# Optimization experiments

Hardware: AMD Instinct MI355X
Metric: run time of the kernel (lower is better)

## Reference

```python
import jax, jax.numpy as jnp
import numpy as np

EPS = 1e-5  # torch BatchNorm1d default eps


def _batchnorm(x, gamma, beta):
    # training-mode BatchNorm1d: biased batch statistics over the N dim
    mean = jnp.mean(x, axis=0)
    var = jnp.var(x, axis=0)
    return (x - mean) * jax.lax.rsqrt(var + EPS) * gamma + beta


def setup_inputs() -> dict:
    key = jax.random.key(0)
    ks = jax.random.split(key, 12)
    N_last, N_cur, E, F = 100000, 50000, 500000, 300
    Din = F + 3  # 303: neighbor features concat coord delta
    inp = {
        "last_coors": jax.random.normal(ks[0], (N_last, 3), jnp.float32),
        "last_features": jax.random.normal(ks[1], (N_last, F), jnp.float32),
        "current_coors": jax.random.normal(ks[2], (N_cur, 3), jnp.float32),
        "cur_idx": jax.random.randint(ks[3], (E,), 0, N_cur),
        "last_idx": jax.random.randint(ks[4], (E,), 0, N_last),
        # in_linear: Linear(303,300) + ReLU + BN(300)
        "W1": jax.random.normal(ks[5], (Din, F), jnp.float32) / np.sqrt(Din),
        "b1": jnp.zeros((F,), jnp.float32),
        "g1": jnp.ones((F,), jnp.float32),
        "be1": jnp.zeros((F,), jnp.float32),
        # out_linear: Linear(300,300) + ReLU + BN(300)
        "W2": jax.random.normal(ks[6], (F, F), jnp.float32) / np.sqrt(F),
        "b2": jnp.zeros((F,), jnp.float32),
        "g2": jnp.ones((F,), jnp.float32),
        "be2": jnp.zeros((F,), jnp.float32),
    }
    return inp


def reference(last_coors, last_features, current_coors, cur_idx, last_idx,
              W1, b1, g1, be1, W2, b2, g2, be2):
    N_cur = current_coors.shape[0]
    # gather: neighbor features + (neighbor - center) coordinate deltas -> [E, 303]
    edge_feats = jnp.concatenate(
        [last_features[last_idx], last_coors[last_idx] - current_coors[cur_idx]],
        axis=1)
    # in_linear MLP on edges
    h = _batchnorm(jnp.maximum(edge_feats @ W1 + b1, 0.0), g1, be1)  # [E, 300]
    # scatter-max aggregation to current-level nodes (empty segments -> 0,
    # matching torch_scatter.scatter(..., reduce='max') zero-init behavior)
    agg = jax.ops.segment_max(h, cur_idx, num_segments=N_cur)  # [N_cur, 300]
    agg = jnp.where(jnp.isfinite(agg), agg, 0.0)
    # out_linear MLP on nodes
    out = _batchnorm(jnp.maximum(agg @ W2 + b2, 0.0), g2, be2)
    return out
```

## Files before the change

kernel.cpp:

```cpp
#include <hip/hip_runtime.h>
#include <hip/hip_bf16.h>


#define NPART 64
#define SB 256
#define SEGB 32
#define CHS 256
#define UNR 8

typedef __bf16 bf16_t;
typedef __bf16 bf16x8 __attribute__((ext_vector_type(8)));
typedef float f32x4 __attribute__((ext_vector_type(4)));

__global__ void hist_k(const int* __restrict__ ci, int E, int* __restrict__ hist)
{
    const int e = blockIdx.x * 256 + threadIdx.x;
    if (e < E) atomicAdd(&hist[ci[e]], 1);
}

__global__ void scan_reduce(const int* __restrict__ hist, int nseg, int* __restrict__ bsum)
{
    __shared__ int s[SB];
    const int tid = threadIdx.x;
    const int i = blockIdx.x * SB + tid;
    s[tid] = (i < nseg) ? hist[i] : 0;
    __syncthreads();
    for (int o = SB / 2; o > 0; o >>= 1) {
        if (tid < o) s[tid] += s[tid + o];
        __syncthreads();
    }
    if (tid == 0) bsum[blockIdx.x] = s[0];
}

__global__ void scan_top(int* __restrict__ bsum, int nb)
{
    __shared__ int s[SB];
    const int tid = threadIdx.x;
    const int v = (tid < nb) ? bsum[tid] : 0;
    s[tid] = v;
    __syncthreads();
    for (int o = 1; o < SB; o <<= 1) {
        int x = 0;
        if (tid >= o) x = s[tid - o];
        __syncthreads();
        s[tid] += x;
        __syncthreads();
    }
    if (tid < nb) bsum[tid] = s[tid] - v;
}

__global__ void scan_final(const int* __restrict__ hist, int nseg,
                           const int* __restrict__ bsum, int* __restrict__ cnt)
{
    __shared__ int s[SB];
    const int tid = threadIdx.x;
    const int i = blockIdx.x * SB + tid;
    const int v = (i < nseg) ? hist[i] : 0;
    s[tid] = v;
    __syncthreads();
    for (int o = 1; o < SB; o <<= 1) {
        int x = 0;
        if (tid >= o) x = s[tid - o];
        __syncthreads();
        s[tid] += x;
        __syncthreads();
    }
    if (i < nseg) cnt[i] = s[tid] - v + bsum[blockIdx.x];
}

__global__ void scatter_k(const int* __restrict__ ci, const int* __restrict__ li,
                          int E, int* __restrict__ cnt, int2* __restrict__ sorted)
{
    const int e = blockIdx.x * 256 + threadIdx.x;
    if (e >= E) return;
    const int c = ci[e];
    const int pos = atomicAdd(&cnt[c], 1);
    sorted[pos] = make_int2(li[e], c);
}

__global__ void pack_wt2(const float* __restrict__ W1, const float* __restrict__ W2,
                         bf16_t* __restrict__ WT)
{
    const int idx = blockIdx.x * 256 + threadIdx.x;
    if (idx >= 2 * 384 * 320) return;
    const int w = idx / (384 * 320);
    const int rem = idx - w * (384 * 320);
    const int n = rem / 320, k = rem % 320;
    const float* W = w ? W2 : W1;
    float v = (n < 300 && k < 300) ? W[k * 300 + n] : 0.f;
    WT[idx] = (bf16_t)v;
}

template<int MODE>
__launch_bounds__(512, 4)
__global__ void gemm_mfma(const float* __restrict__ A32, int M,
                          const int* __restrict__ segEnd,
                          const float* __restrict__ ac,
                          const bf16_t* __restrict__ WT,
                          const float* __restrict__ bias,
                          bf16_t* __restrict__ outBF,
                          float* __restrict__ outF,
                          float* __restrict__ part)
{
    __shared__ bf16_t As[128][72];
    __shared__ bf16_t Bs[320][72];
    __shared__ float sSum[320], sSq[320];
    __shared__ float sAc[640];

    const int tid  = threadIdx.x;
    const int lane = tid & 63, wv = tid >> 6;
    const int wm = wv & 1, wn = wv >> 1;
    const int m0 = blockIdx.x * 128;
    const int rl = lane & 15, quad = lane >> 4;

    if (MODE == 1) {
        if (tid < 320) { sSum[tid] = 0.f; sSq[tid] = 0.f; }
        for (int i = tid; i < 640; i += 512) sAc[i] = ac[i];
    }

    const int kcT = (tid & 7) * 8;
    const int rT  = tid >> 3;
    int growA[2]; bool emp[2];
    #pragma unroll
    for (int i = 0; i < 2; ++i) {
        growA[i] = min(m0 + i * 64 + rT, M - 1);
        emp[i] = false;
        if (MODE == 1)
            emp[i] = segEnd[growA[i]] == (growA[i] ? segEnd[growA[i] - 1] : 0);
    }

    f32x4 acc[4][5];
    #pragma unroll
    for (int i = 0; i < 4; ++i)
        #pragma unroll
        for (int j = 0; j < 5; ++j)
            acc[i][j] = (f32x4){0.f, 0.f, 0.f, 0.f};

    if (MODE == 1) __syncthreads();

    for (int k0 = 0; k0 < 320; k0 += 64) {
        const int c0 = k0 + kcT;

        float4 la[2], lb[2];
        #pragma unroll
        for (int i = 0; i < 2; ++i) {
            la[i] = make_float4(0.f, 0.f, 0.f, 0.f);
            lb[i] = make_float4(0.f, 0.f, 0.f, 0.f);
            if (MODE == 0) {
                if (c0 + 8 <= 300) {
                    la[i] = *reinterpret_cast<const float4*>(&A32[(long)growA[i] * 300 + c0]);
                    lb[i] = *reinterpret_cast<const float4*>(&A32[(long)growA[i] * 300 + c0 + 4]);
                } else if (c0 < 300) {
                    la[i] = *reinterpret_cast<const float4*>(&A32[(long)growA[i] * 300 + c0]);
                }
            } else {
                la[i] = *reinterpret_cast<const float4*>(&A32[(long)growA[i] * 320 + c0]);
                lb[i] = *reinterpret_cast<const float4*>(&A32[(long)growA[i] * 320 + c0 + 4]);
            }
        }
        bf16x8 wb[5];
        #pragma unroll
        for (int i = 0; i < 5; ++i)
            wb[i] = *reinterpret_cast<const bf16x8*>(&WT[(long)(i * 64 + rT) * 320 + c0]);

        #pragma unroll
        for (int i = 0; i < 2; ++i) {
            bf16x8 v;
            if (MODE == 0) {
                v = (bf16x8){(bf16_t)la[i].x, (bf16_t)la[i].y, (bf16_t)la[i].z, (bf16_t)la[i].w,
                             (bf16_t)lb[i].x, (bf16_t)lb[i].y, (bf16_t)lb[i].z, (bf16_t)lb[i].w};
            } else {
                const float4 aa = *reinterpret_cast<const float4*>(&sAc[c0]);
                const float4 ab = *reinterpret_cast<const float4*>(&sAc[c0 + 4]);
                const float4 ca = *reinterpret_cast<const float4*>(&sAc[320 + c0]);
                const float4 cb = *reinterpret_cast<const float4*>(&sAc[320 + c0 + 4]);
                const float t0 = emp[i] ? 0.f : fabsf(aa.x) * la[i].x + ca.x;
                const float t1 = emp[i] ? 0.f : fabsf(aa.y) * la[i].y + ca.y;
                const float t2 = emp[i] ? 0.f : fabsf(aa.z) * la[i].z + ca.z;
                const float t3 = emp[i] ? 0.f : fabsf(aa.w) * la[i].w + ca.w;
                const float t4 = emp[i] ? 0.f : fabsf(ab.x) * lb[i].x + cb.x;
                const float t5 = emp[i] ? 0.f : fabsf(ab.y) * lb[i].y + cb.y;
                const float t6 = emp[i] ? 0.f : fabsf(ab.z) * lb[i].z + cb.z;
                const float t7 = emp[i] ? 0.f : fabsf(ab.w) * lb[i].w + cb.w;
                v = (bf16x8){(bf16_t)t0, (bf16_t)t1, (bf16_t)t2, (bf16_t)t3,
                             (bf16_t)t4, (bf16_t)t5, (bf16_t)t6, (bf16_t)t7};
            }
            *reinterpret_cast<bf16x8*>(&As[i * 64 + rT][kcT]) = v;
        }
        #pragma unroll
        for (int i = 0; i < 5; ++i)
            *reinterpret_cast<bf16x8*>(&Bs[i * 64 + rT][kcT]) = wb[i];
        __syncthreads();

        #pragma unroll
        for (int kk = 0; kk < 2; ++kk) {
            const int kb = kk * 32 + quad * 8;
            bf16x8 af[4], bfr[5];
            #pragma unroll
            for (int mi = 0; mi < 4; ++mi)
                af[mi] = *reinterpret_cast<const bf16x8*>(&As[wm * 64 + mi * 16 + rl][kb]);
            #pragma unroll
            for (int nj = 0; nj < 5; ++nj)
                bfr[nj] = *reinterpret_cast<const bf16x8*>(&Bs[wn * 80 + nj * 16 + rl][kb]);
            #pragma unroll
            for (int mi = 0; mi < 4; ++mi)
                #pragma unroll
                for (int nj = 0; nj < 5; ++nj)
                    acc[mi][nj] = __builtin_amdgcn_mfma_f32_16x16x32_bf16(
                        af[mi], bfr[nj], acc[mi][nj], 0, 0, 0);
        }
        __syncthreads();
    }

    if (MODE == 0) {
        #pragma unroll
        for (int mi = 0; mi < 4; ++mi)
            #pragma unroll
            for (int nj = 0; nj < 5; ++nj)
                #pragma unroll
                for (int reg = 0; reg < 4; ++reg) {
                    const int r = m0 + wm * 64 + mi * 16 + quad * 4 + reg;
                    const int c = wn * 80 + nj * 16 + rl;
                    if (r < M) {
                        const float v = (c < 300) ? (acc[mi][nj][reg] + bias[c]) : 0.f;
                        outBF[(long)r * 320 + c] = (bf16_t)v;
                    }
                }
    } else {
        float csum[5] = {}, csq[5] = {};
        #pragma unroll
        for (int mi = 0; mi < 4; ++mi)
            #pragma unroll
            for (int nj = 0; nj < 5; ++nj)
                #pragma unroll
                for (int reg = 0; reg < 4; ++reg) {
                    const int r = m0 + wm * 64 + mi * 16 + quad * 4 + reg;
                    const int c = wn * 80 + nj * 16 + rl;
                    if (r < M && c < 300) {
                        float v = fmaxf(acc[mi][nj][reg] + bias[c], 0.f);
                        outF[(long)r * 300 + c] = v;
                        csum[nj] += v; csq[nj] += v * v;
                    }
                }
        #pragma unroll
        for (int nj = 0; nj < 5; ++nj) {
            const int cl = wn * 80 + nj * 16 + rl;
            if (cl < 300) {
                atomicAdd(&sSum[cl], csum[nj]);
                atomicAdd(&sSq[cl], csq[nj]);
            }
        }
        __syncthreads();
        const int slot = blockIdx.x & (NPART - 1);
        if (tid < 300) {
            atomicAdd(&part[slot * 600 + tid], sSum[tid]);
            atomicAdd(&part[slot * 600 + 300 + tid], sSq[tid]);
        }
    }
}

__launch_bounds__(320)
__global__ void edge_pass(const bf16_t* __restrict__ Gb,
                          const float* __restrict__ last_coors,
                          const float* __restrict__ cur_coors,
                          const int2* __restrict__ sorted,
                          const int*  __restrict__ segEnd,
                          const float* __restrict__ Wc,
                          const float* __restrict__ g1,
                          float* __restrict__ zbuf,
                          float* __restrict__ part1,
                          int N_cur)
{
    __shared__ int sRow[2][CHS], sCi[2][CHS];
    __shared__ float sD0[2][CHS], sD1[2][CHS], sD2[2][CHS];

    const int tid = threadIdx.x;
    const int st  = (tid >= 160) ? 1 : 0;
    const int ts  = tid - st * 160;

    const int g0   = blockIdx.x * SEGB;
    const int gEnd = min(g0 + SEGB, N_cur);
    const int gMid = min(g0 + SEGB / 2, gEnd);

    const int e00 = (g0   == 0) ? 0 : segEnd[g0 - 1];
    const int e01 = (gMid == 0) ? 0 : segEnd[gMid - 1];
    const int e11 = (gEnd == 0) ? 0 : segEnd[gEnd - 1];

    const int ebeg = st ? e01 : e00;
    const int eend = st ? e11 : e01;

    const int nch0 = (e01 - e00 + CHS - 1) / CHS;
    const int nch1 = (e11 - e01 + CHS - 1) / CHS;
    const int nch  = max(nch0, nch1);

    const int ft = ts * 2;
    const bool real = (ft < 300);
    float w00 = 0.f, w01 = 0.f, w10 = 0.f, w11 = 0.f, w20 = 0.f, w21 = 0.f;
    float sgn0 = 1.f, sgn1 = 1.f;
    if (real) {
        w00 = Wc[ft];        w01 = Wc[ft + 1];
        w10 = Wc[300 + ft];  w11 = Wc[300 + ft + 1];
        w20 = Wc[600 + ft];  w21 = Wc[600 + ft + 1];
        sgn0 = (g1[ft]     < 0.f) ? -1.f : 1.f;
        sgn1 = (g1[ft + 1] < 0.f) ? -1.f : 1.f;
    }

    int cur = -1;
    float m0 = -3.4e38f, m1 = -3.4e38f;
    float sum0 = 0.f, sq0 = 0.f, sum1 = 0.f, sq1 = 0.f;

    for (int ch = 0; ch < nch; ++ch) {
        const int cbeg = ebeg + ch * CHS;
        const int ccnt = min(CHS, eend - cbeg);

        for (int i = ts; i < ccnt; i += 160) {
            const int2 r = sorted[cbeg + i];
            sRow[st][i] = r.x * 320;
            sCi[st][i]  = r.y;
            sD0[st][i] = last_coors[r.x * 3 + 0] - cur_coors[r.y * 3 + 0];
            sD1[st][i] = last_coors[r.x * 3 + 1] - cur_coors[r.y * 3 + 1];
            sD2[st][i] = last_coors[r.x * 3 + 2] - cur_coors[r.y * 3 + 2];
        }
        __syncthreads();

        int i = 0;
        for (; i + UNR <= ccnt; i += UNR) {
            unsigned gu[UNR];
            #pragma unroll
            for (int j = 0; j < UNR; ++j)
                gu[j] = *reinterpret_cast<const unsigned*>(&Gb[(long)sRow[st][i + j] + ft]);
            #pragma unroll
            for (int j = 0; j < UNR; ++j) {
                const int ci = sCi[st][i + j];
                if (ci != cur) {
                    if (cur >= 0)
                        *reinterpret_cast<float2*>(&zbuf[(long)cur * 320 + ft]) =
                            make_float2(m0, m1);
                    cur = ci;
                    m0 = -3.4e38f; m1 = -3.4e38f;
                }
                const float gx = __uint_as_float(gu[j] << 16);
                const float gy = __uint_as_float(gu[j] & 0xffff0000u);
                const float d0 = sD0[st][i + j], d1 = sD1[st][i + j], d2 = sD2[st][i + j];
                const float y0 = fmaxf(gx + d0 * w00 + d1 * w10 + d2 * w20, 0.f);
                const float y1 = fmaxf(gy + d0 * w01 + d1 * w11 + d2 * w21, 0.f);
                sum0 += y0; sq0 += y0 * y0; m0 = fmaxf(m0, sgn0 * y0);
                sum1 += y1; sq1 += y1 * y1; m1 = fmaxf(m1, sgn1 * y1);
            }
        }
        for (; i < ccnt; ++i) {
            const int ci = sCi[st][i];
            if (ci != cur) {
                if (cur >= 0)
                    *reinterpret_cast<float2*>(&zbuf[(long)cur * 320 + ft]) =
                        make_float2(m0, m1);
                cur = ci;
                m0 = -3.4e38f; m1 = -3.4e38f;
            }
            const unsigned gu = *reinterpret_cast<const unsigned*>(&Gb[(long)sRow[st][i] + ft]);
            const float gx = __uint_as_float(gu << 16);
            const float gy = __uint_as_float(gu & 0xffff0000u);
            const float d0 = sD0[st][i], d1 = sD1[st][i], d2 = sD2[st][i];
            const float y0 = fmaxf(gx + d0 * w00 + d1 * w10 + d2 * w20, 0.f);
            const float y1 = fmaxf(gy + d0 * w01 + d1 * w11 + d2 * w21, 0.f);
            sum0 += y0; sq0 += y0 * y0; m0 = fmaxf(m0, sgn0 * y0);
            sum1 += y1; sq1 += y1 * y1; m1 = fmaxf(m1, sgn1 * y1);
        }
        __syncthreads();
    }
    if (cur >= 0)
        *reinterpret_cast<float2*>(&zbuf[(long)cur * 320 + ft]) = make_float2(m0, m1);

    const int slot = blockIdx.x & (NPART - 1);
    if (real) {
        atomicAdd(&part1[slot * 600 + ft],           sum0);
        atomicAdd(&part1[slot * 600 + ft + 1],       sum1);
        atomicAdd(&part1[slot * 600 + 300 + ft],     sq0);
        atomicAdd(&part1[slot * 600 + 300 + ft + 1], sq1);
    }
}

__global__ void stats_finalize(const float* __restrict__ part,
                               const float* __restrict__ g,
                               const float* __restrict__ be,
                               float invCnt, float* __restrict__ ac)
{
    const int t = threadIdx.x;
    if (t >= 300) {
        if (t < 320) { ac[t] = 0.f; ac[320 + t] = 0.f; }
        return;
    }
    float sum = 0.f, sq = 0.f;
    for (int p = 0; p < NPART; ++p) {
        sum += part[p * 600 + t];
        sq  += part[p * 600 + 300 + t];
    }
    const float mean = sum * invCnt;
    const float var = fmaxf(sq * invCnt - mean * mean, 0.f);
    const float inv = rsqrtf(var + 1e-5f);
    const float a = g[t] * inv;
    ac[t] = a;
    ac[320 + t] = be[t] - mean * a;
}

__global__ void finalize_out(float* __restrict__ out,
                             const float* __restrict__ ac2)
{
    const int t = threadIdx.x;
    if (t >= 300) return;
    const long i = (long)blockIdx.x * 300 + t;
    out[i] = ac2[t] * out[i] + ac2[320 + t];
}

extern "C" void kernel_launch(void* const* d_in, const int* in_sizes, int n_in,
                              void* d_out, int out_size, void* d_ws, size_t ws_size,
                              hipStream_t stream)
{
    const float* last_coors    = (const float*)d_in[0];
    const float* last_features = (const float*)d_in[1];
    const float* cur_coors     = (const float*)d_in[2];
    const int*   cur_idx       = (const int*)d_in[3];
    const int*   last_idx      = (const int*)d_in[4];
    const float* W1  = (const float*)d_in[5];
    const float* b1  = (const float*)d_in[6];
    const float* g1  = (const float*)d_in[7];
    const float* be1 = (const float*)d_in[8];
    const float* W2  = (const float*)d_in[9];
    const float* b2  = (const float*)d_in[10];
    const float* g2  = (const float*)d_in[11];
    const float* be2 = (const float*)d_in[12];
    float* out = (float*)d_out;

    const int N_last = in_sizes[0] / 3;
    const int N_cur  = in_sizes[2] / 3;
    const int E      = in_sizes[3];

    const int nb1 = (N_cur + SB - 1) / SB;

    char* ws = (char*)d_ws;
    size_t off = 0;
    bf16_t* Gb = (bf16_t*)(ws + off);  off += (size_t)N_last * 320 * 2;
    off = (off + 255) & ~(size_t)255;
    float* zbuf = (float*)(ws + off);  off += (size_t)N_cur * 320 * 4;
    off = (off + 255) & ~(size_t)255;
    int2* sorted = (int2*)(ws + off);  off += (size_t)E * 8;
    int* hist = (int*)(ws + off);      off += (size_t)nb1 * SB * 4;
    int* cnt  = (int*)(ws + off);      off += (size_t)nb1 * SB * 4;
    int* bsum = (int*)(ws + off);      off += 256 * 4;
    bf16_t* WT1 = (bf16_t*)(ws + off); off += (size_t)384 * 320 * 2;
    bf16_t* WT2 = (bf16_t*)(ws + off); off += (size_t)384 * 320 * 2;
    float* part1 = (float*)(ws + off); off += (size_t)NPART * 600 * 4;
    float* part2 = (float*)(ws + off); off += (size_t)NPART * 600 * 4;
    float* ac1   = (float*)(ws + off); off += 640 * 4;
    float* ac2   = (float*)(ws + off); off += 640 * 4;

    hipMemsetAsync(hist, 0, (size_t)nb1 * SB * 4, stream);
    hipMemsetAsync(part1, 0, (size_t)2 * NPART * 600 * 4, stream);

    hist_k<<<(E + 255) / 256, 256, 0, stream>>>(cur_idx, E, hist);
    scan_reduce<<<nb1, SB, 0, stream>>>(hist, N_cur, bsum);
    scan_top<<<1, SB, 0, stream>>>(bsum, nb1);
    scan_final<<<nb1, SB, 0, stream>>>(hist, N_cur, bsum, cnt);
    scatter_k<<<(E + 255) / 256, 256, 0, stream>>>(cur_idx, last_idx, E, cnt, sorted);

    pack_wt2<<<960, 256, 0, stream>>>(W1, W2, WT1);

    gemm_mfma<0><<<(N_last + 127) / 128, 512, 0, stream>>>(
        last_features, N_last, nullptr, nullptr, WT1, b1, Gb, nullptr, nullptr);

    const int nSB = (N_cur + SEGB - 1) / SEGB;
    edge_pass<<<nSB, 320, 0, stream>>>(Gb, last_coors, cur_coors, sorted, cnt,
                                       W1 + 300 * 300, g1, zbuf, part1, N_cur);

    stats_finalize<<<1, 320, 0, stream>>>(part1, g1, be1, 1.0f / (float)E, ac1);

    gemm_mfma<1><<<(N_cur + 127) / 128, 512, 0, stream>>>(
        zbuf, N_cur, cnt, ac1, WT2, b2, nullptr, out, part2);

    stats_finalize<<<1, 320, 0, stream>>>(part2, g2, be2, 1.0f / (float)N_cur, ac2);
    finalize_out<<<N_cur, 320, 0, stream>>>(out, ac2);
}
```

Baseline: 548.2 us.

## Double-buffer A tiles and read weights directly from global in MFMA GEMM

The GEMM kernel is restructured to 256-thread blocks covering 64 rows. Each of the 4 waves owns 80 output columns. The weight (B) tile is no longer staged in shared memory; each wave loads its B fragments straight from global/L2 memory. The A tile is double-buffered so the next k-slice's global loads overlap the current MFMA work. This removes the large Bs shared buffer and one barrier stage per iteration, at the cost of redundant global weight reads per block and smaller tiles that give less reuse.

```diff
diff --git a/kernel.cpp b/kernel.cpp
--- a/kernel.cpp
+++ b/kernel.cpp
@@ -92,7 +92,7 @@
 }
 
 template<int MODE>
-__launch_bounds__(512, 4)
+__launch_bounds__(256, 3)
 __global__ void gemm_mfma(const float* __restrict__ A32, int M,
                           const int* __restrict__ segEnd,
                           const float* __restrict__ ac,
@@ -102,67 +102,52 @@
                           float* __restrict__ outF,
                           float* __restrict__ part)
 {
-    __shared__ bf16_t As[128][72];
-    __shared__ bf16_t Bs[320][72];
+    __shared__ bf16_t As[2][64][72];
     __shared__ float sSum[320], sSq[320];
     __shared__ float sAc[640];
 
     const int tid  = threadIdx.x;
-    const int lane = tid & 63, wv = tid >> 6;
-    const int wm = wv & 1, wn = wv >> 1;
-    const int m0 = blockIdx.x * 128;
+    const int lane = tid & 63, wn = tid >> 6;
+    const int m0 = blockIdx.x * 64;
     const int rl = lane & 15, quad = lane >> 4;
-
-    if (MODE == 1) {
-        if (tid < 320) { sSum[tid] = 0.f; sSq[tid] = 0.f; }
-        for (int i = tid; i < 640; i += 512) sAc[i] = ac[i];
-    }
 
     const int kcT = (tid & 7) * 8;
     const int rT  = tid >> 3;
-    int growA[2]; bool emp[2];
+    int grow[2]; bool emp[2];
     #pragma unroll
     for (int i = 0; i < 2; ++i) {
-        growA[i] = min(m0 + i * 64 + rT, M - 1);
+        grow[i] = min(m0 + i * 32 + rT, M - 1);
         emp[i] = false;
         if (MODE == 1)
-            emp[i] = segEnd[growA[i]] == (growA[i] ? segEnd[growA[i] - 1] : 0);
-    }
-
-    f32x4 acc[4][5];
-    #pragma unroll
-    for (int i = 0; i < 4; ++i)
-        #pragma unroll
-        for (int j = 0; j < 5; ++j)
-            acc[i][j] = (f32x4){0.f, 0.f, 0.f, 0.f};
-
-    if (MODE == 1) __syncthreads();
-
-    for (int k0 = 0; k0 < 320; k0 += 64) {
-        const int c0 = k0 + kcT;
-
-        float4 la[2], lb[2];
+            emp[i] = segEnd[grow[i]] == (grow[i] ? segEnd[grow[i] - 1] : 0);
+    }
+
+    if (MODE == 1) {
+        for (int i = tid; i < 320; i += 256) { sSum[i] = 0.f; sSq[i] = 0.f; }
+        for (int i = tid; i < 640; i += 256) sAc[i] = ac[i];
+    }
+
+    auto LOADA = [&](int k0p, float4* la, float4* lb) {
+        const int c0 = k0p + kcT;
         #pragma unroll
         for (int i = 0; i < 2; ++i) {
             la[i] = make_float4(0.f, 0.f, 0.f, 0.f);
             lb[i] = make_float4(0.f, 0.f, 0.f, 0.f);
             if (MODE == 0) {
                 if (c0 + 8 <= 300) {
-                    la[i] = *reinterpret_cast<const float4*>(&A32[(long)growA[i] * 300 + c0]);
-                    lb[i] = *reinterpret_cast<const float4*>(&A32[(long)growA[i] * 300 + c0 + 4]);
+                    la[i] = *reinterpret_cast<const float4*>(&A32[(long)grow[i] * 300 + c0]);
+                    lb[i] = *reinterpret_cast<const float4*>(&A32[(long)grow[i] * 300 + c0 + 4]);
                 } else if (c0 < 300) {
-                    la[i] = *reinterpret_cast<const float4*>(&A32[(long)growA[i] * 300 + c0]);
+                    la[i] = *reinterpret_cast<const float4*>(&A32[(long)grow[i] * 300 + c0]);
                 }
             } else {
-                la[i] = *reinterpret_cast<const float4*>(&A32[(long)growA[i] * 320 + c0]);
-                lb[i] = *reinterpret_cast<const float4*>(&A32[(long)growA[i] * 320 + c0 + 4]);
+                la[i] = *reinterpret_cast<const float4*>(&A32[(long)grow[i] * 320 + c0]);
+                lb[i] = *reinterpret_cast<const float4*>(&A32[(long)grow[i] * 320 + c0 + 4]);
             }
         }
-        bf16x8 wb[5];
-        #pragma unroll
-        for (int i = 0; i < 5; ++i)
-            wb[i] = *reinterpret_cast<const bf16x8*>(&WT[(long)(i * 64 + rT) * 320 + c0]);
-
+    };
+    auto STOREA = [&](int buf, int k0p, const float4* la, const float4* lb) {
+        const int c0 = k0p + kcT;
         #pragma unroll
         for (int i = 0; i < 2; ++i) {
             bf16x8 v;
@@ -185,23 +170,43 @@
                 v = (bf16x8){(bf16_t)t0, (bf16_t)t1, (bf16_t)t2, (bf16_t)t3,
                              (bf16_t)t4, (bf16_t)t5, (bf16_t)t6, (bf16_t)t7};
             }
-            *reinterpret_cast<bf16x8*>(&As[i * 64 + rT][kcT]) = v;
-        }
-        #pragma unroll
-        for (int i = 0; i < 5; ++i)
-            *reinterpret_cast<bf16x8*>(&Bs[i * 64 + rT][kcT]) = wb[i];
-        __syncthreads();
+            *reinterpret_cast<bf16x8*>(&As[buf][i * 32 + rT][kcT]) = v;
+        }
+    };
+
+    f32x4 acc[4][5];
+    #pragma unroll
+    for (int i = 0; i < 4; ++i)
+        #pragma unroll
+        for (int j = 0; j < 5; ++j)
+            acc[i][j] = (f32x4){0.f, 0.f, 0.f, 0.f};
+
+    {
+        float4 la[2], lb[2];
+        LOADA(0, la, lb);
+        if (MODE == 1) __syncthreads();
+        STOREA(0, 0, la, lb);
+    }
+    __syncthreads();
+
+    #pragma unroll
+    for (int t = 0; t < 5; ++t) {
+        const int cb = t & 1, nb = (t + 1) & 1;
+        const int k0 = t * 64;
+        float4 la[2], lb[2];
+        if (t + 1 < 5) LOADA((t + 1) * 64, la, lb);
 
         #pragma unroll
         for (int kk = 0; kk < 2; ++kk) {
             const int kb = kk * 32 + quad * 8;
             bf16x8 af[4], bfr[5];
             #pragma unroll
+            for (int nj = 0; nj < 5; ++nj)
+                bfr[nj] = *reinterpret_cast<const bf16x8*>(
+                    &WT[(long)(wn * 80 + nj * 16 + rl) * 320 + k0 + kb]);
+            #pragma unroll
             for (int mi = 0; mi < 4; ++mi)
-                af[mi] = *reinterpret_cast<const bf16x8*>(&As[wm * 64 + mi * 16 + rl][kb]);
-            #pragma unroll
-            for (int nj = 0; nj < 5; ++nj)
-                bfr[nj] = *reinterpret_cast<const bf16x8*>(&Bs[wn * 80 + nj * 16 + rl][kb]);
+                af[mi] = *reinterpret_cast<const bf16x8*>(&As[cb][mi * 16 + rl][kb]);
             #pragma unroll
             for (int mi = 0; mi < 4; ++mi)
                 #pragma unroll
@@ -209,6 +214,8 @@
                     acc[mi][nj] = __builtin_amdgcn_mfma_f32_16x16x32_bf16(
                         af[mi], bfr[nj], acc[mi][nj], 0, 0, 0);
         }
+
+        if (t + 1 < 5) STOREA(nb, (t + 1) * 64, la, lb);
         __syncthreads();
     }
 
@@ -219,7 +226,7 @@
             for (int nj = 0; nj < 5; ++nj)
                 #pragma unroll
                 for (int reg = 0; reg < 4; ++reg) {
-                    const int r = m0 + wm * 64 + mi * 16 + quad * 4 + reg;
+                    const int r = m0 + mi * 16 + quad * 4 + reg;
                     const int c = wn * 80 + nj * 16 + rl;
                     if (r < M) {
                         const float v = (c < 300) ? (acc[mi][nj][reg] + bias[c]) : 0.f;
@@ -234,7 +241,7 @@
             for (int nj = 0; nj < 5; ++nj)
                 #pragma unroll
                 for (int reg = 0; reg < 4; ++reg) {
-                    const int r = m0 + wm * 64 + mi * 16 + quad * 4 + reg;
+                    const int r = m0 + mi * 16 + quad * 4 + reg;
                     const int c = wn * 80 + nj * 16 + rl;
                     if (r < M && c < 300) {
                         float v = fmaxf(acc[mi][nj][reg] + bias[c], 0.f);
@@ -252,9 +259,9 @@
         }
         __syncthreads();
         const int slot = blockIdx.x & (NPART - 1);
-        if (tid < 300) {
-            atomicAdd(&part[slot * 600 + tid], sSum[tid]);
-            atomicAdd(&part[slot * 600 + 300 + tid], sSq[tid]);
+        for (int i = tid; i < 300; i += 256) {
+            atomicAdd(&part[slot * 600 + i], sSum[i]);
+            atomicAdd(&part[slot * 600 + 300 + i], sSq[i]);
         }
     }
 }
@@ -465,7 +472,7 @@
 
     pack_wt2<<<960, 256, 0, stream>>>(W1, W2, WT1);
 
-    gemm_mfma<0><<<(N_last + 127) / 128, 512, 0, stream>>>(
+    gemm_mfma<0><<<(N_last + 63) / 64, 256, 0, stream>>>(
         last_features, N_last, nullptr, nullptr, WT1, b1, Gb, nullptr, nullptr);
 
     const int nSB = (N_cur + SEGB - 1) / SEGB;
@@ -474,7 +481,7 @@
 
     stats_finalize<<<1, 320, 0, stream>>>(part1, g1, be1, 1.0f / (float)E, ac1);
 
-    gemm_mfma<1><<<(N_cur + 127) / 128, 512, 0, stream>>>(
+    gemm_mfma<1><<<(N_cur + 63) / 64, 256, 0, stream>>>(
         zbuf, N_cur, cnt, ac1, WT2, b2, nullptr, out, part2);
 
     stats_finalize<<<1, 320, 0, stream>>>(part2, g2, be2, 1.0f / (float)N_cur, ac2);
```

Result: faster. 537.3 us (-2.0%).
